# Kernel optimization log

Hardware: AMD Instinct MI355X
Metric: run time of the kernel (lower is better)

Reference implementation:

```python
import jax, jax.numpy as jnp
import numpy as np

L, H, E, FFN, V, BLOCK = 8, 16, 1024, 4096, 32000, 2048
D = E // H  # head dim = 64
EPS = 1e-5
STD = 0.02

def _ln(x, g, b):
    m = jnp.mean(x, axis=-1, keepdims=True)
    v = jnp.var(x, axis=-1, keepdims=True)
    return (x - m) * jax.lax.rsqrt(v + EPS) * g + b

def setup_inputs() -> dict:
    key = jax.random.key(0)
    ks = jax.random.split(key, 12)
    n = lambda k, shape: (jax.random.normal(k, shape, dtype=jnp.float32) * STD)
    return {
        "idx": jax.random.randint(ks[0], (2, 2048), 0, V),
        "tok_emb": n(ks[1], (V, E)),
        "pos_emb": n(ks[2], (BLOCK, E)),
        # attention weights stored [in, out] so we use x @ W
        "wq": n(ks[3], (L, E, E)),
        "wk": n(ks[4], (L, E, E)),
        "wv": n(ks[5], (L, E, E)),
        "wo": n(ks[6], (L, E, E)),
        "bo": jnp.zeros((L, E), jnp.float32),
        "w1": n(ks[7], (L, E, FFN)),
        "b1": jnp.zeros((L, FFN), jnp.float32),
        "w2": n(ks[8], (L, FFN, E)),
        "b2": jnp.zeros((L, E), jnp.float32),
        "ln1_g": jnp.ones((L, E), jnp.float32),
        "ln1_b": jnp.zeros((L, E), jnp.float32),
        "ln2_g": jnp.ones((L, E), jnp.float32),
        "ln2_b": jnp.zeros((L, E), jnp.float32),
        "lnf_g": jnp.ones((E,), jnp.float32),
        "lnf_b": jnp.zeros((E,), jnp.float32),
    }

def reference(idx, tok_emb, pos_emb, wq, wk, wv, wo, bo, w1, b1, w2, b2,
              ln1_g, ln1_b, ln2_g, ln2_b, lnf_g, lnf_b):
    B, T = idx.shape
    x = tok_emb[idx] + pos_emb[:T]  # [B,T,E]
    causal = jnp.tril(jnp.ones((T, T), dtype=bool))
    scale = 1.0 / np.sqrt(D)

    def step(x, p):
        (wq_, wk_, wv_, wo_, bo_, w1_, b1_, w2_, b2_,
         g1, be1, g2, be2) = p
        h = _ln(x, g1, be1)
        q = (h @ wq_).reshape(B, T, H, D)
        k = (h @ wk_).reshape(B, T, H, D)
        v = (h @ wv_).reshape(B, T, H, D)
        scores = jnp.einsum('bthd,bshd->bhts', q, k) * scale  # [B,H,T,T]
        scores = jnp.where(causal, scores, -jnp.inf)
        w = jax.nn.softmax(scores, axis=-1)
        attn = jnp.einsum('bhts,bshd->bthd', w, v).reshape(B, T, E)
        x = x + attn @ wo_ + bo_
        h2 = _ln(x, g2, be2)
        x = x + jax.nn.relu(h2 @ w1_ + b1_) @ w2_ + b2_
        return x, None

    x, _ = jax.lax.scan(step, x, (wq, wk, wv, wo, bo, w1, b1, w2, b2,
                                  ln1_g, ln1_b, ln2_g, ln2_b))
    x = _ln(x, lnf_g, lnf_b)
    logits = x @ tok_emb.T  # tied weights
    return logits
```

## Files before the change

kernel.cpp:

```cpp
#include <hip/hip_runtime.h>
#include <hip/hip_bf16.h>
#include <cstdint>
#include <cstddef>

#define LAYERS   8
#define HEADS    16
#define EMB      1024
#define FFND     4096
#define VOCAB    32000
#define SEQ      2048
#define NBATCH   2
#define MROWS    (NBATCH*SEQ)
#define HDIM     64
#define QKVSTR   3072
#define LN_EPS   1e-5f

typedef __hip_bfloat16 bf16;
typedef short short8 __attribute__((ext_vector_type(8)));
typedef float f32x4  __attribute__((ext_vector_type(4)));

__device__ __forceinline__ void async_copy16(const bf16* g, bf16* l) {
  __builtin_amdgcn_global_load_lds(
      (const __attribute__((address_space(1))) void*)g,
      (__attribute__((address_space(3))) void*)l, 16, 0, 0);
}

__device__ __forceinline__ uint32_t bfbits(float x) {
  __hip_bfloat16 h = __float2bfloat16(x);
  return (uint32_t)reinterpret_cast<uint16_t&>(h);
}

struct __align__(8) B4 { bf16 a, b, c, d; };

__global__ void k_f32_to_bf16(const float* __restrict__ in, bf16* __restrict__ out, long n4) {
  long i = (long)blockIdx.x * blockDim.x + threadIdx.x;
  const long stride = (long)gridDim.x * blockDim.x;
  for (; i < n4; i += stride) {
    float4 v = reinterpret_cast<const float4*>(in)[i];
    B4 o;
    o.a = __float2bfloat16(v.x);
    o.b = __float2bfloat16(v.y);
    o.c = __float2bfloat16(v.z);
    o.d = __float2bfloat16(v.w);
    reinterpret_cast<B4*>(out)[i] = o;
  }
}

__global__ void k_embed(const int* __restrict__ idx, const float* __restrict__ tok,
                        const float* __restrict__ pos, float* __restrict__ x) {
  const int row  = blockIdx.x;
  const int tpos = row & (SEQ - 1);
  const int token = idx[row];
  const float4* te = (const float4*)(tok + (long)token * EMB);
  const float4* pe = (const float4*)(pos + (long)tpos * EMB);
  float4* xo = (float4*)(x + (long)row * EMB);
  for (int i = threadIdx.x; i < EMB / 4; i += blockDim.x) {
    float4 a = te[i], b = pe[i];
    a.x += b.x; a.y += b.y; a.z += b.z; a.w += b.w;
    xo[i] = a;
  }
}

__global__ void k_transpose_w(const float* __restrict__ in, bf16* __restrict__ out,
                              int K, int N) {
  __shared__ float tile[32][33];
  const int n0 = blockIdx.x * 32, k0 = blockIdx.y * 32;
  const int tx = threadIdx.x, ty = threadIdx.y;
  for (int i = 0; i < 32; i += 8)
    tile[ty + i][tx] = in[(long)(k0 + ty + i) * N + n0 + tx];
  __syncthreads();
  for (int i = 0; i < 32; i += 8)
    out[(long)(n0 + ty + i) * K + k0 + tx] = __float2bfloat16(tile[tx][ty + i]);
}

__global__ void k_transpose_w4(const float* __restrict__ wq, const float* __restrict__ wk,
                               const float* __restrict__ wv, const float* __restrict__ wo,
                               bf16* __restrict__ qkvT, bf16* __restrict__ woT) {
  __shared__ float tile[32][33];
  const float* in;
  bf16* out;
  switch (blockIdx.z) {
    case 0:  in = wq; out = qkvT;               break;
    case 1:  in = wk; out = qkvT + EMB * EMB;   break;
    case 2:  in = wv; out = qkvT + 2 * EMB * EMB; break;
    default: in = wo; out = woT;                break;
  }
  const int n0 = blockIdx.x * 32, k0 = blockIdx.y * 32;
  const int tx = threadIdx.x, ty = threadIdx.y;
  for (int i = 0; i < 32; i += 8)
    tile[ty + i][tx] = in[(long)(k0 + ty + i) * EMB + n0 + tx];
  __syncthreads();
  for (int i = 0; i < 32; i += 8)
    out[(long)(n0 + ty + i) * EMB + k0 + tx] = __float2bfloat16(tile[tx][ty + i]);
}

__global__ void k_transpose_v(const bf16* __restrict__ v, int vstr, bf16* __restrict__ vt) {
  __shared__ bf16 tile[32][33];
  const int bh = blockIdx.z;
  const int b = bh >> 4, h = bh & 15;
  const int t0 = blockIdx.x * 32, d0 = blockIdx.y * 32;
  const int tx = threadIdx.x, ty = threadIdx.y;
  for (int i = 0; i < 32; i += 8)
    tile[ty + i][tx] = v[(long)(b * SEQ + t0 + ty + i) * vstr + h * HDIM + d0 + tx];
  __syncthreads();
  for (int i = 0; i < 32; i += 8)
    vt[(long)(bh * HDIM + d0 + ty + i) * SEQ + t0 + tx] = tile[tx][ty + i];
}

__global__ __launch_bounds__(256)
void k_layernorm(const float* __restrict__ x, const float* __restrict__ g,
                 const float* __restrict__ b, bf16* __restrict__ out) {
  const long row = blockIdx.x;
  const float* xr = x + row * EMB;
  const int t = threadIdx.x;
  float xv[4];
  float s = 0.f, sq = 0.f;
#pragma unroll
  for (int i = 0; i < 4; i++) {
    xv[i] = xr[t + i * 256];
    s += xv[i];
    sq += xv[i] * xv[i];
  }
#pragma unroll
  for (int m = 1; m < 64; m <<= 1) { s += __shfl_xor(s, m); sq += __shfl_xor(sq, m); }
  __shared__ float rs_[4], rq_[4];
  const int wid = t >> 6;
  if ((t & 63) == 0) { rs_[wid] = s; rq_[wid] = sq; }
  __syncthreads();
  s  = rs_[0] + rs_[1] + rs_[2] + rs_[3];
  sq = rq_[0] + rq_[1] + rq_[2] + rq_[3];
  const float mean = s * (1.f / EMB);
  const float var  = sq * (1.f / EMB) - mean * mean;
  const float rstd = rsqrtf(var + LN_EPS);
#pragma unroll
  for (int i = 0; i < 4; i++) {
    const int c = t + i * 256;
    out[row * EMB + c] = __float2bfloat16((xv[i] - mean) * rstd * g[c] + b[c]);
  }
}

template<int MODE>
__global__ __launch_bounds__(512, 2)
void gemm256(const bf16* __restrict__ A, const bf16* __restrict__ Bt,
             int M, int N, int K,
             bf16* __restrict__ outB, float* __restrict__ outF,
             const float* __restrict__ bias) {
  extern __shared__ __align__(16) char smem[];
  char* const smA = smem;
  char* const smB = smem + 65536;

  const int t    = threadIdx.x;
  const int lane = t & 63;
  const int wid  = t >> 6;
  const int wr   = wid >> 2;
  const int wc   = wid & 3;
  const int lrow = lane & 15;
  const int ks16 = (lane >> 4) * 16;
  const int rswz = (lrow & 7) << 4;

  int lin = blockIdx.x * gridDim.y + blockIdx.y;
  { const int nwg = gridDim.x * gridDim.y; const int per = nwg >> 3;
    lin = (lin & 7) * per + (lin >> 3); }
  const int gx8  = gridDim.x * 8;
  const int half = lin / gx8;
  const int rem  = lin - half * gx8;
  const long bm  = (long)(half * 8 + (rem & 7)) * 256;
  const long bn  = (long)(rem >> 3) * 256;
  const int NT = K >> 6;

  const int row0 = wid * 8 + (lane >> 3);
  const int col0 = ((lane & 7) ^ (lane >> 3)) * 8;
  const int row1 = row0 + 64;
  const int dst0 = wid * 1024;
  const int dst1 = 8192 + wid * 1024;
  const bf16* const gA = A  + bm * K;
  const bf16* const gB = Bt + bn * K;

  auto STG = [&](char* ring, const bf16* g_, int tile, int h) {
    char* slot = ring + (((tile << 1) + h) & 3) * 16384;
    const bf16* sb = g_ + ((long)h * 128) * K + (long)tile * 64;
    async_copy16(sb + (long)row0 * K + col0, (bf16*)(slot + dst0));
    async_copy16(sb + (long)row1 * K + col0, (bf16*)(slot + dst1));
  };
  auto LDA8 = [&](int u, int m, int kk) -> short8 {
    const int off = (m * 16 + lrow) * 128 + ((kk * 64 + ks16) ^ rswz);
    return *reinterpret_cast<const short8*>(smA + (((u << 1) + wr) & 3) * 16384 + off);
  };
  auto LDB8 = [&](int u, int n, int kk) -> short8 {
    const int off = ((wc & 1) * 64 + n * 16 + lrow) * 128 + ((kk * 64 + ks16) ^ rswz);
    return *reinterpret_cast<const short8*>(smB + (((u << 1) + (wc >> 1)) & 3) * 16384 + off);
  };
#define MF(a_, b_, c_) __builtin_amdgcn_mfma_f32_16x16x32_bf16(a_, b_, c_, 0, 0, 0)

  f32x4 acc[8][4] = {};

  STG(smB, gB, 0, 0); STG(smB, gB, 0, 1);
  STG(smA, gA, 0, 0); STG(smA, gA, 0, 1);
  STG(smB, gB, 1, 0); STG(smB, gB, 1, 1);
  asm volatile("s_waitcnt vmcnt(4)" ::: "memory");
  __builtin_amdgcn_s_barrier();

  short8 bq[4][2];
  for (int u = 0; u < NT; u++) {
#pragma unroll
    for (int n = 0; n < 4; n++) { bq[n][0] = LDB8(u, n, 0); bq[n][1] = LDB8(u, n, 1); }
    short8 a0 = LDA8(u, 0, 0), a1 = LDA8(u, 0, 1), a2 = LDA8(u, 1, 0), a3 = LDA8(u, 1, 1);
    if (u + 1 < NT) STG(smA, gA, u + 1, 0);
    __builtin_amdgcn_s_barrier();
    asm volatile("s_waitcnt lgkmcnt(0)" ::: "memory");
    __builtin_amdgcn_sched_barrier(0);
    __builtin_amdgcn_s_setprio(1);
#pragma unroll
    for (int n = 0; n < 4; n++) {
      acc[0][n] = MF(a0, bq[n][0], acc[0][n]); acc[0][n] = MF(a1, bq[n][1], acc[0][n]);
      acc[1][n] = MF(a2, bq[n][0], acc[1][n]); acc[1][n] = MF(a3, bq[n][1], acc[1][n]);
    }
    __builtin_amdgcn_s_setprio(0);
    __builtin_amdgcn_s_barrier();

    a0 = LDA8(u, 2, 0); a1 = LDA8(u, 2, 1); a2 = LDA8(u, 3, 0); a3 = LDA8(u, 3, 1);
    if (u + 1 < NT) STG(smA, gA, u + 1, 1);
    __builtin_amdgcn_s_barrier();
    asm volatile("s_waitcnt lgkmcnt(0)" ::: "memory");
    __builtin_amdgcn_sched_barrier(0);
    __builtin_amdgcn_s_setprio(1);
#pragma unroll
    for (int n = 0; n < 4; n++) {
      acc[2][n] = MF(a0, bq[n][0], acc[2][n]); acc[2][n] = MF(a1, bq[n][1], acc[2][n]);
      acc[3][n] = MF(a2, bq[n][0], acc[3][n]); acc[3][n] = MF(a3, bq[n][1], acc[3][n]);
    }
    __builtin_amdgcn_s_setprio(0);
    __builtin_amdgcn_s_barrier();

    a0 = LDA8(u, 4, 0); a1 = LDA8(u, 4, 1); a2 = LDA8(u, 5, 0); a3 = LDA8(u, 5, 1);
    if (u + 2 < NT) STG(smB, gB, u + 2, 0);
    __builtin_amdgcn_s_barrier();
    asm volatile("s_waitcnt lgkmcnt(0)" ::: "memory");
    __builtin_amdgcn_sched_barrier(0);
    __builtin_amdgcn_s_setprio(1);
#pragma unroll
    for (int n = 0; n < 4; n++) {
      acc[4][n] = MF(a0, bq[n][0], acc[4][n]); acc[4][n] = MF(a1, bq[n][1], acc[4][n]);
      acc[5][n] = MF(a2, bq[n][0], acc[5][n]); acc[5][n] = MF(a3, bq[n][1], acc[5][n]);
    }
    __builtin_amdgcn_s_setprio(0);
    __builtin_amdgcn_s_barrier();

    a0 = LDA8(u, 6, 0); a1 = LDA8(u, 6, 1); a2 = LDA8(u, 7, 0); a3 = LDA8(u, 7, 1);
    if (u + 2 < NT) STG(smB, gB, u + 2, 1);
    __builtin_amdgcn_s_barrier();
    asm volatile("s_waitcnt lgkmcnt(0)" ::: "memory");
    __builtin_amdgcn_sched_barrier(0);
    __builtin_amdgcn_s_setprio(1);
#pragma unroll
    for (int n = 0; n < 4; n++) {
      acc[6][n] = MF(a0, bq[n][0], acc[6][n]); acc[6][n] = MF(a1, bq[n][1], acc[6][n]);
      acc[7][n] = MF(a2, bq[n][0], acc[7][n]); acc[7][n] = MF(a3, bq[n][1], acc[7][n]);
    }
    __builtin_amdgcn_s_setprio(0);
    if (u + 2 < NT) { asm volatile("s_waitcnt vmcnt(4)" ::: "memory"); }
    else            { asm volatile("s_waitcnt vmcnt(0)" ::: "memory"); }
    __builtin_amdgcn_s_barrier();
  }

  const long rb = bm + wr * 128 + (lane >> 4) * 4;
  const long cb = bn + wc * 64 + lrow;
#pragma unroll
  for (int m = 0; m < 8; m++) {
#pragma unroll
    for (int n = 0; n < 4; n++) {
      const long col = cb + n * 16;
#pragma unroll
      for (int r = 0; r < 4; r++) {
        const long row = rb + m * 16 + r;
        float v = acc[m][n][r];
        if (MODE == 0) {
          outB[row * N + col] = __float2bfloat16(v);
        } else if (MODE == 2) {
          v += bias[col];
          outB[row * N + col] = __float2bfloat16(v > 0.f ? v : 0.f);
        } else {
          outF[row * N + col] = v;
        }
      }
    }
  }
#undef MF
}

#define BM 128
#define BN 128
#define BK 32

__global__ __launch_bounds__(256)
void gemm_bt(const bf16* __restrict__ A, const bf16* __restrict__ Bt,
             int M, int N, int K,
             float* __restrict__ outF, const float* __restrict__ bias) {
  __shared__ __align__(16) bf16 lA[BM * BK];
  __shared__ __align__(16) bf16 lB[BN * BK];
  const int t    = threadIdx.x;
  const int lane = t & 63;
  const int wid  = t >> 6;
  const int wr   = wid >> 1;
  const int wc   = wid & 1;
  const long bm  = (long)blockIdx.y * BM;
  const long bn  = (long)blockIdx.x * BN;

  f32x4 acc[4][4] = {};

  const long arow = t >> 2;
  const int  acol = (((t & 3) ^ ((t >> 2) & 3)) * 8);
  const bf16* gA = A  + (bm + arow) * K + acol;
  const bf16* gB = Bt + (bn + arow) * K + acol;
  bf16* dA = lA + wid * 512;
  bf16* dB = lB + wid * 512;
  const long astep = 64L * K;

  for (int k0 = 0; k0 < K; k0 += BK) {
    async_copy16(gA + k0,         dA);
    async_copy16(gA + k0 + astep, dA + 2048);
    async_copy16(gB + k0,         dB);
    async_copy16(gB + k0 + astep, dB + 2048);
    __syncthreads();

    const int ksel = (((lane >> 4) ^ (lane & 3)) * 8);
    short8 af[4], bfv[4];
#pragma unroll
    for (int i = 0; i < 4; i++) {
      af[i]  = *reinterpret_cast<const short8*>(&lA[(wr * 64 + i * 16 + (lane & 15)) * BK + ksel]);
      bfv[i] = *reinterpret_cast<const short8*>(&lB[(wc * 64 + i * 16 + (lane & 15)) * BK + ksel]);
    }
#pragma unroll
    for (int i = 0; i < 4; i++)
#pragma unroll
      for (int j = 0; j < 4; j++)
        acc[i][j] = __builtin_amdgcn_mfma_f32_16x16x32_bf16(af[i], bfv[j], acc[i][j], 0, 0, 0);
    __syncthreads();
  }

  const long rbase = bm + wr * 64 + (lane >> 4) * 4;
  const long cbase = bn + wc * 64 + (lane & 15);
#pragma unroll
  for (int i = 0; i < 4; i++) {
#pragma unroll
    for (int j = 0; j < 4; j++) {
      const long col = cbase + j * 16;
#pragma unroll
      for (int r = 0; r < 4; r++) {
        const long row = rbase + i * 16 + r;
        outF[row * N + col] += acc[i][j][r] + bias[col];
      }
    }
  }
}

__global__ __launch_bounds__(256)
void k_attn(const bf16* __restrict__ qkv, const bf16* __restrict__ vt, bf16* __restrict__ o) {
  const int qt = gridDim.x - 1 - blockIdx.x;
  const int bh = blockIdx.y;
  const int b  = bh >> 4;
  const int h  = bh & 15;
  const int t0b = qt * 64;
  const int tid = threadIdx.x;
  const int w    = tid >> 6;
  const int lane = tid & 63;
  const int lg = lane >> 4;
  const int li = lane & 15;
  const int t0w = t0b + w * 16;

  __shared__ __align__(16) bf16 Kl[2][64 * 64];
  __shared__ __align__(16) bf16 Vl[2][64 * 64];
  __shared__ __align__(16) bf16 Pl[4][16 * 64];

  const bf16* qbase = qkv + (long)(b * SEQ) * QKVSTR + h * HDIM;
  const bf16* kbase = qkv + (long)(b * SEQ) * QKVSTR + EMB + h * HDIM;
  const bf16* vbase = vt + (long)bh * HDIM * SEQ;

  short8 qf[2];
  {
    const bf16* qrow = qbase + (long)(t0w + li) * QKVSTR;
    qf[0] = *reinterpret_cast<const short8*>(&qrow[lg * 8]);
    qf[1] = *reinterpret_cast<const short8*>(&qrow[32 + lg * 8]);
  }

  f32x4 oacc[4] = {};
  float mrow = -1e30f, lrow = 0.f;

  const int nkt = t0b >> 6;
  const int l8  = lane >> 3;
  const int sl8 = ((lane & 7) ^ l8) * 8;

  char* const Pw = (char*)&Pl[w][0];
  const int pswz = (li & 7) << 4;

#pragma unroll
  for (int sh = 0; sh < 2; sh++) {
    const int r = sh * 32 + w * 8 + l8;
    async_copy16(kbase + (long)r * QKVSTR + sl8, &Kl[0][(sh * 32 + w * 8) * 64]);
    async_copy16(vbase + (long)r * SEQ + sl8,    &Vl[0][(sh * 32 + w * 8) * 64]);
  }
  __syncthreads();

  int cur = 0;
  for (int kt = 0; kt <= nkt; kt++) {
    const int s0 = kt * 64;
    if (kt < nkt) {
      const int s0n = s0 + 64;
      bf16* Kn = &Kl[cur ^ 1][0];
      bf16* Vn = &Vl[cur ^ 1][0];
#pragma unroll
      for (int sh = 0; sh < 2; sh++) {
        const int r = sh * 32 + w * 8 + l8;
        async_copy16(kbase + (long)(s0n + r) * QKVSTR + sl8, Kn + (sh * 32 + w * 8) * 64);
        async_copy16(vbase + (long)r * SEQ + s0n + sl8,      Vn + (sh * 32 + w * 8) * 64);
      }
    }

    f32x4 s[4] = {};
#pragma unroll
    for (int kk = 0; kk < 2; kk++)
#pragma unroll
      for (int sf = 0; sf < 4; sf++) {
        const short8 kf = *reinterpret_cast<const short8*>(
            &Kl[cur][(sf * 16 + li) * 64 + ((((kk << 2) | lg) ^ (li & 7)) * 8)]);
        s[sf] = __builtin_amdgcn_mfma_f32_16x16x32_bf16(kf, qf[kk], s[sf], 0, 0, 0);
      }

    const bool diag = (kt == nkt);
#pragma unroll
    for (int sf = 0; sf < 4; sf++)
#pragma unroll
      for (int r = 0; r < 4; r++) {
        float val = s[sf][r] * 0.18033688011112042f;
        if (diag && (s0 + sf * 16 + lg * 4 + r > t0w + li)) val = -1e30f;
        s[sf][r] = val;
      }

    float mx = -1e30f;
#pragma unroll
    for (int sf = 0; sf < 4; sf++)
      mx = fmaxf(mx, fmaxf(fmaxf(s[sf][0], s[sf][1]), fmaxf(s[sf][2], s[sf][3])));
    mx = fmaxf(mx, __shfl_xor(mx, 16));
    mx = fmaxf(mx, __shfl_xor(mx, 32));
    const float mnew = fmaxf(mrow, mx);
    const float alpha = exp2f(mrow - mnew);
    mrow = mnew;
    float rs = 0.f;
#pragma unroll
    for (int sf = 0; sf < 4; sf++)
#pragma unroll
      for (int r = 0; r < 4; r++) {
        const float pv = exp2f(s[sf][r] - mnew);
        s[sf][r] = pv;
        rs += pv;
      }
    rs += __shfl_xor(rs, 16);
    rs += __shfl_xor(rs, 32);
    lrow = lrow * alpha + rs;
#pragma unroll
    for (int d = 0; d < 4; d++)
#pragma unroll
      for (int r = 0; r < 4; r++) oacc[d][r] *= alpha;

#pragma unroll
    for (int sf = 0; sf < 4; sf++) {
      uint2 pw2;
      pw2.x = (bfbits(s[sf][1]) << 16) | bfbits(s[sf][0]);
      pw2.y = (bfbits(s[sf][3]) << 16) | bfbits(s[sf][2]);
      *reinterpret_cast<uint2*>(Pw + li * 128 + ((sf * 32 + lg * 8) ^ pswz)) = pw2;
    }
#pragma unroll
    for (int kk = 0; kk < 2; kk++) {
      const short8 pb = *reinterpret_cast<const short8*>(
          Pw + li * 128 + ((kk * 64 + lg * 16) ^ pswz));
#pragma unroll
      for (int d = 0; d < 4; d++) {
        const short8 vf = *reinterpret_cast<const short8*>(
            &Vl[cur][(d * 16 + li) * 64 + ((((kk << 2) | lg) ^ (li & 7)) * 8)]);
        oacc[d] = __builtin_amdgcn_mfma_f32_16x16x32_bf16(vf, pb, oacc[d], 0, 0, 0);
      }
    }

    __syncthreads();
    cur ^= 1;
  }

  const float inv = 1.f / lrow;
  bf16* orow = o + (long)(b * SEQ + t0w + li) * EMB + h * HDIM;
#pragma unroll
  for (int d = 0; d < 4; d++) {
    uint2 ow;
    ow.x = (bfbits(oacc[d][1] * inv) << 16) | bfbits(oacc[d][0] * inv);
    ow.y = (bfbits(oacc[d][3] * inv) << 16) | bfbits(oacc[d][2] * inv);
    *reinterpret_cast<uint2*>(&orow[d * 16 + lg * 4]) = ow;
  }
}

extern "C" void kernel_launch(void* const* d_in, const int* in_sizes, int n_in,
                              void* d_out, int out_size, void* d_ws, size_t ws_size,
                              hipStream_t stream) {
  (void)in_sizes; (void)n_in; (void)out_size; (void)ws_size;
  const int*   idx = (const int*)  d_in[0];
  const float* tok = (const float*)d_in[1];
  const float* pos = (const float*)d_in[2];
  const float* wq  = (const float*)d_in[3];
  const float* wk  = (const float*)d_in[4];
  const float* wv  = (const float*)d_in[5];
  const float* wo  = (const float*)d_in[6];
  const float* bo  = (const float*)d_in[7];
  const float* w1  = (const float*)d_in[8];
  const float* b1  = (const float*)d_in[9];
  const float* w2  = (const float*)d_in[10];
  const float* b2  = (const float*)d_in[11];
  const float* g1  = (const float*)d_in[12];
  const float* be1 = (const float*)d_in[13];
  const float* g2  = (const float*)d_in[14];
  const float* be2 = (const float*)d_in[15];
  const float* gf  = (const float*)d_in[16];
  const float* bef = (const float*)d_in[17];
  float* out = (float*)d_out;

  (void)hipFuncSetAttribute((const void*)gemm256<0>, hipFuncAttributeMaxDynamicSharedMemorySize, 131072);
  (void)hipFuncSetAttribute((const void*)gemm256<2>, hipFuncAttributeMaxDynamicSharedMemorySize, 131072);
  (void)hipFuncSetAttribute((const void*)gemm256<3>, hipFuncAttributeMaxDynamicSharedMemorySize, 131072);

  char* p = (char*)d_ws;
  auto take = [&p](size_t bytes) { char* r = p; p += (bytes + 255) & ~(size_t)255; return r; };
  float* xf   = (float*)take((size_t)MROWS * EMB * 4);
  bf16*  hb   = (bf16*) take((size_t)MROWS * EMB * 2);
  bf16*  qkvb = (bf16*) take((size_t)MROWS * QKVSTR * 2);
  bf16*  vtb  = (bf16*) take((size_t)MROWS * EMB * 2);
  bf16*  ab   = (bf16*) take((size_t)MROWS * EMB * 2);
  bf16*  fb   = (bf16*) take((size_t)MROWS * FFND * 2);
  bf16*  wqkvT= (bf16*) take((size_t)QKVSTR * EMB * 2);
  bf16*  woT  = (bf16*) take((size_t)EMB * EMB * 2);
  bf16*  w1T  = (bf16*) take((size_t)FFND * EMB * 2);
  bf16*  w2T  = (bf16*) take((size_t)EMB * FFND * 2);
  bf16*  tokT = (bf16*) take((size_t)VOCAB * EMB * 2);

  k_f32_to_bf16<<<2048, 256, 0, stream>>>(tok, tokT, (long)VOCAB * EMB / 4);
  k_embed<<<MROWS, 256, 0, stream>>>(idx, tok, pos, xf);

  const dim3 tb(32, 8);

  for (int l = 0; l < LAYERS; l++) {
    const size_t we = (size_t)l * EMB * EMB;
    const size_t wfo = (size_t)l * EMB * FFND;
    k_transpose_w4<<<dim3(EMB / 32, EMB / 32, 4), tb, 0, stream>>>(
        wq + we, wk + we, wv + we, wo + we, wqkvT, woT);
    k_transpose_w<<<dim3(FFND / 32, EMB / 32),  tb, 0, stream>>>(w1 + wfo, w1T, EMB,  FFND);
    k_transpose_w<<<dim3(EMB / 32,  FFND / 32), tb, 0, stream>>>(w2 + wfo, w2T, FFND, EMB);

    k_layernorm<<<MROWS, 256, 0, stream>>>(xf, g1 + l * EMB, be1 + l * EMB, hb);
    gemm256<0><<<dim3(QKVSTR / 256, MROWS / 256), 512, 131072, stream>>>(
        hb, wqkvT, MROWS, QKVSTR, EMB, qkvb, nullptr, nullptr);
    k_transpose_v<<<dim3(SEQ / 32, HDIM / 32, NBATCH * HEADS), tb, 0, stream>>>(qkvb + 2 * EMB, QKVSTR, vtb);
    k_attn<<<dim3(SEQ / 64, NBATCH * HEADS), 256, 0, stream>>>(qkvb, vtb, ab);
    gemm_bt<<<dim3(EMB / BN, MROWS / BM), 256, 0, stream>>>(ab, woT, MROWS, EMB, EMB, xf, bo + l * EMB);
    k_layernorm<<<MROWS, 256, 0, stream>>>(xf, g2 + l * EMB, be2 + l * EMB, hb);
    gemm256<2><<<dim3(FFND / 256, MROWS / 256), 512, 131072, stream>>>(
        hb, w1T, MROWS, FFND, EMB, fb, nullptr, b1 + l * FFND);
    gemm_bt<<<dim3(EMB / BN, MROWS / BM), 256, 0, stream>>>(fb, w2T, MROWS, EMB, FFND, xf, b2 + l * EMB);
  }

  k_layernorm<<<MROWS, 256, 0, stream>>>(xf, gf, bef, hb);
  gemm256<3><<<dim3(VOCAB / 256, MROWS / 256), 512, 131072, stream>>>(
      hb, tokT, MROWS, VOCAB, EMB, nullptr, out, nullptr);
}
```

Baseline: 3.013 ms.

## Double-buffer gemm_bt LDS tiles and double attention query tile per block

gemm_bt now double-buffers its A/B LDS tiles and issues the next K-slab's async loads before computing on the current one, so global-load latency overlaps with MFMA work. The attention kernel processes 128 query rows per block (32 per wave, as two 16-row fragments) instead of 64, so each K/V tile loaded into LDS is reused across twice as many queries. The costs are more LDS, more registers per wave, a grid half as large (fewer blocks for load balance on the causal triangle), and masking applied on the last two key tiles.

```diff
diff --git a/kernel.cpp b/kernel.cpp
--- a/kernel.cpp
+++ b/kernel.cpp
@@ -296,8 +296,8 @@
 void gemm_bt(const bf16* __restrict__ A, const bf16* __restrict__ Bt,
              int M, int N, int K,
              float* __restrict__ outF, const float* __restrict__ bias) {
-  __shared__ __align__(16) bf16 lA[BM * BK];
-  __shared__ __align__(16) bf16 lB[BN * BK];
+  __shared__ __align__(16) bf16 lA[2][BM * BK];
+  __shared__ __align__(16) bf16 lB[2][BN * BK];
   const int t    = threadIdx.x;
   const int lane = t & 63;
   const int wid  = t >> 6;
@@ -312,23 +312,28 @@
   const int  acol = (((t & 3) ^ ((t >> 2) & 3)) * 8);
   const bf16* gA = A  + (bm + arow) * K + acol;
   const bf16* gB = Bt + (bn + arow) * K + acol;
-  bf16* dA = lA + wid * 512;
-  bf16* dB = lB + wid * 512;
   const long astep = 64L * K;
 
+  auto STGBT = [&](int buf, int k0) {
+    async_copy16(gA + k0,         &lA[buf][wid * 512]);
+    async_copy16(gA + k0 + astep, &lA[buf][wid * 512 + 2048]);
+    async_copy16(gB + k0,         &lB[buf][wid * 512]);
+    async_copy16(gB + k0 + astep, &lB[buf][wid * 512 + 2048]);
+  };
+
+  STGBT(0, 0);
+  __syncthreads();
+
+  int cur = 0;
   for (int k0 = 0; k0 < K; k0 += BK) {
-    async_copy16(gA + k0,         dA);
-    async_copy16(gA + k0 + astep, dA + 2048);
-    async_copy16(gB + k0,         dB);
-    async_copy16(gB + k0 + astep, dB + 2048);
-    __syncthreads();
+    if (k0 + BK < K) STGBT(cur ^ 1, k0 + BK);
 
     const int ksel = (((lane >> 4) ^ (lane & 3)) * 8);
     short8 af[4], bfv[4];
 #pragma unroll
     for (int i = 0; i < 4; i++) {
-      af[i]  = *reinterpret_cast<const short8*>(&lA[(wr * 64 + i * 16 + (lane & 15)) * BK + ksel]);
-      bfv[i] = *reinterpret_cast<const short8*>(&lB[(wc * 64 + i * 16 + (lane & 15)) * BK + ksel]);
+      af[i]  = *reinterpret_cast<const short8*>(&lA[cur][(wr * 64 + i * 16 + (lane & 15)) * BK + ksel]);
+      bfv[i] = *reinterpret_cast<const short8*>(&lB[cur][(wc * 64 + i * 16 + (lane & 15)) * BK + ksel]);
     }
 #pragma unroll
     for (int i = 0; i < 4; i++)
@@ -336,6 +341,7 @@
       for (int j = 0; j < 4; j++)
         acc[i][j] = __builtin_amdgcn_mfma_f32_16x16x32_bf16(af[i], bfv[j], acc[i][j], 0, 0, 0);
     __syncthreads();
+    cur ^= 1;
   }
 
   const long rbase = bm + wr * 64 + (lane >> 4) * 4;
@@ -360,33 +366,34 @@
   const int bh = blockIdx.y;
   const int b  = bh >> 4;
   const int h  = bh & 15;
-  const int t0b = qt * 64;
+  const int t0b = qt * 128;
   const int tid = threadIdx.x;
   const int w    = tid >> 6;
   const int lane = tid & 63;
   const int lg = lane >> 4;
   const int li = lane & 15;
-  const int t0w = t0b + w * 16;
+  const int t0w = t0b + w * 32;
 
   __shared__ __align__(16) bf16 Kl[2][64 * 64];
   __shared__ __align__(16) bf16 Vl[2][64 * 64];
-  __shared__ __align__(16) bf16 Pl[4][16 * 64];
+  __shared__ __align__(16) bf16 Pl[4][32 * 64];
 
   const bf16* qbase = qkv + (long)(b * SEQ) * QKVSTR + h * HDIM;
   const bf16* kbase = qkv + (long)(b * SEQ) * QKVSTR + EMB + h * HDIM;
   const bf16* vbase = vt + (long)bh * HDIM * SEQ;
 
-  short8 qf[2];
-  {
-    const bf16* qrow = qbase + (long)(t0w + li) * QKVSTR;
-    qf[0] = *reinterpret_cast<const short8*>(&qrow[lg * 8]);
-    qf[1] = *reinterpret_cast<const short8*>(&qrow[32 + lg * 8]);
-  }
-
-  f32x4 oacc[4] = {};
-  float mrow = -1e30f, lrow = 0.f;
-
-  const int nkt = t0b >> 6;
+  short8 qf[2][2];
+#pragma unroll
+  for (int f = 0; f < 2; f++) {
+    const bf16* qrow = qbase + (long)(t0w + f * 16 + li) * QKVSTR;
+    qf[f][0] = *reinterpret_cast<const short8*>(&qrow[lg * 8]);
+    qf[f][1] = *reinterpret_cast<const short8*>(&qrow[32 + lg * 8]);
+  }
+
+  f32x4 oacc[2][4] = {};
+  float mrow[2] = {-1e30f, -1e30f}, lrow[2] = {0.f, 0.f};
+
+  const int nkt = (t0b >> 6) + 1;
   const int l8  = lane >> 3;
   const int sl8 = ((lane & 7) ^ l8) * 8;
 
@@ -416,68 +423,78 @@
       }
     }
 
-    f32x4 s[4] = {};
+    f32x4 s[2][4] = {};
 #pragma unroll
     for (int kk = 0; kk < 2; kk++)
 #pragma unroll
       for (int sf = 0; sf < 4; sf++) {
         const short8 kf = *reinterpret_cast<const short8*>(
             &Kl[cur][(sf * 16 + li) * 64 + ((((kk << 2) | lg) ^ (li & 7)) * 8)]);
-        s[sf] = __builtin_amdgcn_mfma_f32_16x16x32_bf16(kf, qf[kk], s[sf], 0, 0, 0);
+        s[0][sf] = __builtin_amdgcn_mfma_f32_16x16x32_bf16(kf, qf[0][kk], s[0][sf], 0, 0, 0);
+        s[1][sf] = __builtin_amdgcn_mfma_f32_16x16x32_bf16(kf, qf[1][kk], s[1][sf], 0, 0, 0);
       }
 
-    const bool diag = (kt == nkt);
-#pragma unroll
-    for (int sf = 0; sf < 4; sf++)
-#pragma unroll
-      for (int r = 0; r < 4; r++) {
-        float val = s[sf][r] * 0.18033688011112042f;
-        if (diag && (s0 + sf * 16 + lg * 4 + r > t0w + li)) val = -1e30f;
-        s[sf][r] = val;
+    const bool diag = (kt >= nkt - 1);
+#pragma unroll
+    for (int f = 0; f < 2; f++)
+#pragma unroll
+      for (int sf = 0; sf < 4; sf++)
+#pragma unroll
+        for (int r = 0; r < 4; r++) {
+          float val = s[f][sf][r] * 0.18033688011112042f;
+          if (diag && (s0 + sf * 16 + lg * 4 + r > t0w + f * 16 + li)) val = -1e30f;
+          s[f][sf][r] = val;
+        }
+
+#pragma unroll
+    for (int f = 0; f < 2; f++) {
+      float mx = -1e30f;
+#pragma unroll
+      for (int sf = 0; sf < 4; sf++)
+        mx = fmaxf(mx, fmaxf(fmaxf(s[f][sf][0], s[f][sf][1]), fmaxf(s[f][sf][2], s[f][sf][3])));
+      mx = fmaxf(mx, __shfl_xor(mx, 16));
+      mx = fmaxf(mx, __shfl_xor(mx, 32));
+      const float mnew = fmaxf(mrow[f], mx);
+      const float alpha = exp2f(mrow[f] - mnew);
+      mrow[f] = mnew;
+      float rs = 0.f;
+#pragma unroll
+      for (int sf = 0; sf < 4; sf++)
+#pragma unroll
+        for (int r = 0; r < 4; r++) {
+          const float pv = exp2f(s[f][sf][r] - mnew);
+          s[f][sf][r] = pv;
+          rs += pv;
+        }
+      rs += __shfl_xor(rs, 16);
+      rs += __shfl_xor(rs, 32);
+      lrow[f] = lrow[f] * alpha + rs;
+#pragma unroll
+      for (int d = 0; d < 4; d++)
+#pragma unroll
+        for (int r = 0; r < 4; r++) oacc[f][d][r] *= alpha;
+
+#pragma unroll
+      for (int sf = 0; sf < 4; sf++) {
+        uint2 pw2;
+        pw2.x = (bfbits(s[f][sf][1]) << 16) | bfbits(s[f][sf][0]);
+        pw2.y = (bfbits(s[f][sf][3]) << 16) | bfbits(s[f][sf][2]);
+        *reinterpret_cast<uint2*>(Pw + (f * 16 + li) * 128 + ((sf * 32 + lg * 8) ^ pswz)) = pw2;
       }
-
-    float mx = -1e30f;
-#pragma unroll
-    for (int sf = 0; sf < 4; sf++)
-      mx = fmaxf(mx, fmaxf(fmaxf(s[sf][0], s[sf][1]), fmaxf(s[sf][2], s[sf][3])));
-    mx = fmaxf(mx, __shfl_xor(mx, 16));
-    mx = fmaxf(mx, __shfl_xor(mx, 32));
-    const float mnew = fmaxf(mrow, mx);
-    const float alpha = exp2f(mrow - mnew);
-    mrow = mnew;
-    float rs = 0.f;
-#pragma unroll
-    for (int sf = 0; sf < 4; sf++)
-#pragma unroll
-      for (int r = 0; r < 4; r++) {
-        const float pv = exp2f(s[sf][r] - mnew);
-        s[sf][r] = pv;
-        rs += pv;
-      }
-    rs += __shfl_xor(rs, 16);
-    rs += __shfl_xor(rs, 32);
-    lrow = lrow * alpha + rs;
-#pragma unroll
-    for (int d = 0; d < 4; d++)
-#pragma unroll
-      for (int r = 0; r < 4; r++) oacc[d][r] *= alpha;
-
-#pragma unroll
-    for (int sf = 0; sf < 4; sf++) {
-      uint2 pw2;
-      pw2.x = (bfbits(s[sf][1]) << 16) | bfbits(s[sf][0]);
-      pw2.y = (bfbits(s[sf][3]) << 16) | bfbits(s[sf][2]);
-      *reinterpret_cast<uint2*>(Pw + li * 128 + ((sf * 32 + lg * 8) ^ pswz)) = pw2;
-    }
+    }
+
 #pragma unroll
     for (int kk = 0; kk < 2; kk++) {
-      const short8 pb = *reinterpret_cast<const short8*>(
+      const short8 pb0 = *reinterpret_cast<const short8*>(
           Pw + li * 128 + ((kk * 64 + lg * 16) ^ pswz));
+      const short8 pb1 = *reinterpret_cast<const short8*>(
+          Pw + (16 + li) * 128 + ((kk * 64 + lg * 16) ^ pswz));
 #pragma unroll
       for (int d = 0; d < 4; d++) {
         const short8 vf = *reinterpret_cast<const short8*>(
             &Vl[cur][(d * 16 + li) * 64 + ((((kk << 2) | lg) ^ (li & 7)) * 8)]);
-        oacc[d] = __builtin_amdgcn_mfma_f32_16x16x32_bf16(vf, pb, oacc[d], 0, 0, 0);
+        oacc[0][d] = __builtin_amdgcn_mfma_f32_16x16x32_bf16(vf, pb0, oacc[0][d], 0, 0, 0);
+        oacc[1][d] = __builtin_amdgcn_mfma_f32_16x16x32_bf16(vf, pb1, oacc[1][d], 0, 0, 0);
       }
     }
 
@@ -485,14 +502,17 @@
     cur ^= 1;
   }
 
-  const float inv = 1.f / lrow;
-  bf16* orow = o + (long)(b * SEQ + t0w + li) * EMB + h * HDIM;
-#pragma unroll
-  for (int d = 0; d < 4; d++) {
-    uint2 ow;
-    ow.x = (bfbits(oacc[d][1] * inv) << 16) | bfbits(oacc[d][0] * inv);
-    ow.y = (bfbits(oacc[d][3] * inv) << 16) | bfbits(oacc[d][2] * inv);
-    *reinterpret_cast<uint2*>(&orow[d * 16 + lg * 4]) = ow;
+#pragma unroll
+  for (int f = 0; f < 2; f++) {
+    const float inv = 1.f / lrow[f];
+    bf16* orow = o + (long)(b * SEQ + t0w + f * 16 + li) * EMB + h * HDIM;
+#pragma unroll
+    for (int d = 0; d < 4; d++) {
+      uint2 ow;
+      ow.x = (bfbits(oacc[f][d][1] * inv) << 16) | bfbits(oacc[f][d][0] * inv);
+      ow.y = (bfbits(oacc[f][d][3] * inv) << 16) | bfbits(oacc[f][d][2] * inv);
+      *reinterpret_cast<uint2*>(&orow[d * 16 + lg * 4]) = ow;
+    }
   }
 }
 
@@ -555,7 +575,7 @@
     gemm256<0><<<dim3(QKVSTR / 256, MROWS / 256), 512, 131072, stream>>>(
         hb, wqkvT, MROWS, QKVSTR, EMB, qkvb, nullptr, nullptr);
     k_transpose_v<<<dim3(SEQ / 32, HDIM / 32, NBATCH * HEADS), tb, 0, stream>>>(qkvb + 2 * EMB, QKVSTR, vtb);
-    k_attn<<<dim3(SEQ / 64, NBATCH * HEADS), 256, 0, stream>>>(qkvb, vtb, ab);
+    k_attn<<<dim3(SEQ / 128, NBATCH * HEADS), 256, 0, stream>>>(qkvb, vtb, ab);
     gemm_bt<<<dim3(EMB / BN, MROWS / BM), 256, 0, stream>>>(ab, woT, MROWS, EMB, EMB, xf, bo + l * EMB);
     k_layernorm<<<MROWS, 256, 0, stream>>>(xf, g2 + l * EMB, be2 + l * EMB, hb);
     gemm256<2><<<dim3(FFND / 256, MROWS / 256), 512, 131072, stream>>>(
```

Measured after the change: 3.020 ms. About the same (+0.2%).
